# Performance work log

Measured on AMD Instinct MI355X. Metric: run time of the kernel, lower is better.

Reference implementation:

```python
import jax, jax.numpy as jnp
import numpy as np

N, E, E3, DIM = 25000, 50000, 40000, 64


def setup_inputs() -> dict:
    key = jax.random.key(0)
    ks = jax.random.split(key, 16)
    def g(k, shape, scale=0.1):
        return jax.random.normal(k, shape, jnp.float32) * scale
    return {
        "x": jax.random.normal(ks[0], (N, 8), jnp.float32),
        "edge_attr": jax.random.uniform(ks[1], (E, 19), dtype=jnp.float32),
        "edge_attr3": jax.random.uniform(ks[2], (E3, 8), dtype=jnp.float32),
        "edge_index": jax.random.randint(ks[3], (2, E), 0, N),
        "edge_index3": jax.random.randint(ks[4], (2, E3), 0, N),
        "W_node": g(ks[5], (8, DIM)), "b_node": jnp.zeros((DIM,), jnp.float32),
        "W_ea": g(ks[6], (19, 12)), "b_ea": jnp.zeros((12,), jnp.float32),
        "W_e1": g(ks[7], (12, 128)), "b_e1": jnp.zeros((128,), jnp.float32),
        "W_e2": g(ks[8], (128, DIM * DIM), 0.01), "b_e2": jnp.zeros((DIM * DIM,), jnp.float32),
        "conv_bias": jnp.zeros((DIM,), jnp.float32),
        "W_ih": g(ks[9], (3 * DIM, DIM)), "b_ih": jnp.zeros((3 * DIM,), jnp.float32),
        "W_hh": g(ks[10], (3 * DIM, DIM)), "b_hh": jnp.zeros((3 * DIM,), jnp.float32),
        "W_l1": g(ks[11], (DIM + 8, 128)), "b_l1": jnp.zeros((128,), jnp.float32),
        "W_l2": g(ks[12], (128, 1)), "b_l2": jnp.zeros((1,), jnp.float32),
    }


def _forward(x, edge_attr, edge_attr3,
             W_node, b_node, W_ea, b_ea, W_e1, b_e1, W_e2, b_e2, conv_bias,
             W_ih, b_ih, W_hh, b_hh, W_l1, b_l1, W_l2, b_l2,
             edge_index, edge_index3):
    dim = W_node.shape[1]
    n = x.shape[0]
    out = jax.nn.relu(x @ W_node + b_node)                      # [N, dim]
    ea = jax.nn.relu(edge_attr @ W_ea + b_ea)                   # [E, 12]
    # edge MLP -> per-edge dim x dim weight matrices (same for all 3 conv calls)
    Wedge = (jax.nn.relu(ea @ W_e1 + b_e1) @ W_e2 + b_e2).reshape(-1, dim, dim)  # [E, dim, dim]
    src, dst = edge_index[0], edge_index[1]
    ones = jnp.ones((src.shape[0],), x.dtype)
    cnt = jnp.maximum(jax.ops.segment_sum(ones, dst, num_segments=n), 1.0)  # [N]
    h = out
    for _ in range(3):
        msg = jnp.einsum('ed,edf->ef', out[src], Wedge)                     # per-edge GEMV
        agg = jax.ops.segment_sum(msg, dst, num_segments=n) / cnt[:, None]  # scatter-mean
        m = jax.nn.relu(agg + conv_bias)
        # single-step GRU (PyTorch gate order: r, z, n)
        gi = m @ W_ih.T + b_ih
        gh = h @ W_hh.T + b_hh
        ir, iz, inn = jnp.split(gi, 3, axis=-1)
        hr, hz, hn = jnp.split(gh, 3, axis=-1)
        r = jax.nn.sigmoid(ir + hr)
        z = jax.nn.sigmoid(iz + hz)
        ng = jnp.tanh(inn + r * hn)
        h = (1.0 - z) * ng + z * h
        out = h
    pair = (out[edge_index3[0]] + out[edge_index3[1]]) * 0.5    # mean over the 2 endpoints
    yhat = jnp.concatenate([pair, edge_attr3], axis=1)          # [E3, dim+8]
    yhat = jax.nn.relu(yhat @ W_l1 + b_l1) @ W_l2 + b_l2        # [E3, 1]
    return yhat[:, 0]


def reference(x, edge_attr, edge_attr3, edge_index, edge_index3,
              W_node, b_node, W_ea, b_ea, W_e1, b_e1, W_e2, b_e2, conv_bias,
              W_ih, b_ih, W_hh, b_hh, W_l1, b_l1, W_l2, b_l2):
    return _forward(x, edge_attr, edge_attr3,
                    W_node, b_node, W_ea, b_ea, W_e1, b_e1, W_e2, b_e2, conv_bias,
                    W_ih, b_ih, W_hh, b_hh, W_l1, b_l1, W_l2, b_l2,
                    edge_index, edge_index3)
```

## Files before the change

### kernel.cpp

```cpp
#include <hip/hip_runtime.h>

typedef unsigned short u16;
typedef unsigned int u32;
typedef __attribute__((ext_vector_type(8))) short short8v;
typedef __attribute__((ext_vector_type(4))) float float4v;

__device__ __forceinline__ float sigm(float x) { return 1.0f / (1.0f + __expf(-x)); }
__device__ __forceinline__ u16 f2bf(float f) {
  u32 u = __float_as_uint(f);
  u32 r = (u + 0x7fffu + ((u >> 16) & 1u)) >> 16;
  return (u16)r;
}
__device__ __forceinline__ float bf2f(u16 w) { return __uint_as_float(((u32)w) << 16); }

__global__ void k_zero_i(int* __restrict__ p, int n) {
  int i = blockIdx.x * blockDim.x + threadIdx.x;
  if (i < n) p[i] = 0;
}

__global__ void k_cnt(const int* __restrict__ dst, int* __restrict__ cnt, int E) {
  int e = blockIdx.x * blockDim.x + threadIdx.x;
  if (e < E) atomicAdd(&cnt[dst[e]], 1);
}

__global__ void k_scan1(const int* __restrict__ cnt, int* __restrict__ bsum, int N) {
  __shared__ int ws[4];
  int t = threadIdx.x;
  int i = blockIdx.x * 256 + t;
  int v = (i < N) ? cnt[i] : 0;
  int s = v;
  for (int off = 1; off < 64; off <<= 1) s += __shfl_xor(s, off);
  int wid = t >> 6, lane = t & 63;
  if (lane == 0) ws[wid] = s;
  __syncthreads();
  if (t == 0) bsum[blockIdx.x] = ws[0] + ws[1] + ws[2] + ws[3];
}

__global__ void k_scan2(int* __restrict__ bsum, int* __restrict__ row, int nb, int N) {
  __shared__ int s[256];
  int t = threadIdx.x;
  if (t < nb) s[t] = bsum[t];
  __syncthreads();
  if (t == 0) {
    int run = 0;
    for (int i = 0; i < nb; ++i) { int x = s[i]; s[i] = run; run += x; }
    row[N] = run;
  }
  __syncthreads();
  if (t < nb) bsum[t] = s[t];
}

__global__ void k_scan3(const int* __restrict__ cnt, const int* __restrict__ bsum,
                        int* __restrict__ row, int* __restrict__ cursor, int N) {
  __shared__ int ws[4];
  int t = threadIdx.x;
  int i = blockIdx.x * 256 + t;
  int v = (i < N) ? cnt[i] : 0;
  int lane = t & 63, wid = t >> 6;
  int incl = v;
  for (int off = 1; off < 64; off <<= 1) {
    int u = __shfl_up(incl, off);
    if (lane >= off) incl += u;
  }
  if (lane == 63) ws[wid] = incl;
  __syncthreads();
  int woff = bsum[blockIdx.x];
  for (int w = 0; w < wid; ++w) woff += ws[w];
  int excl = woff + incl - v;
  if (i < N) { row[i] = excl; cursor[i] = excl; }
}

__global__ void k_pos(const int* __restrict__ dst, int* __restrict__ cursor,
                      int* __restrict__ pos, int E) {
  int e = blockIdx.x * blockDim.x + threadIdx.x;
  if (e < E) pos[e] = atomicAdd(&cursor[dst[e]], 1);
}

__global__ void k_node(const float* __restrict__ x, const float* __restrict__ Wn,
                       const float* __restrict__ bn, float* __restrict__ h, int N) {
  int tid = blockIdx.x * blockDim.x + threadIdx.x;
  if (tid >= N * 64) return;
  int n = tid >> 6, f = tid & 63;
  float acc = bn[f];
  for (int k = 0; k < 8; ++k) acc += x[(size_t)n * 8 + k] * Wn[k * 64 + f];
  h[tid] = fmaxf(acc, 0.0f);
}

__global__ __launch_bounds__(256) void k_edge_mlp(
    const float* __restrict__ ea_in, const float* __restrict__ Wea,
    const float* __restrict__ bea, const float* __restrict__ We1,
    const float* __restrict__ be1, u16* __restrict__ Ahi, int E) {
  __shared__ float att[2][19];
  __shared__ float ea[2][12];
  int half = threadIdx.x >> 7;
  int t = threadIdx.x & 127;
  int e = blockIdx.x * 2 + half;
  bool real = (e < E);
  int ee = real ? e : E - 1;
  if (t < 19) att[half][t] = ea_in[(size_t)ee * 19 + t];
  __syncthreads();
  if (t < 12) {
    float a = bea[t];
#pragma unroll
    for (int k = 0; k < 19; ++k) a += att[half][k] * Wea[k * 12 + t];
    ea[half][t] = fmaxf(a, 0.0f);
  }
  __syncthreads();
  float a = be1[t];
#pragma unroll
  for (int j = 0; j < 12; ++j) a += ea[half][j] * We1[j * 128 + t];
  if (real) Ahi[(size_t)e * 128 + t] = f2bf(fmaxf(a, 0.0f));
}

__global__ void k_pack_b(const float* __restrict__ W2, u16* __restrict__ Bph) {
  int tid = blockIdx.x * blockDim.x + threadIdx.x;
  if (tid >= 128 * 4096) return;
  int j = tid & 7;
  int lane = (tid >> 3) & 63;
  int nt = (tid >> 9) & 3;
  int ks = (tid >> 11) & 3;
  int d = tid >> 13;
  int c = lane & 15, q = lane >> 4;
  int k = ks * 32 + q * 8 + j;
  int n = d * 64 + nt * 16 + c;
  Bph[tid] = f2bf(W2[(size_t)k * 4096 + n]);
}

__global__ void k_prep_wtf(const float* __restrict__ Wih, const float* __restrict__ Whh,
                           u16* __restrict__ WpI, u16* __restrict__ WpH) {
  int tid = blockIdx.x * blockDim.x + threadIdx.x;
  if (tid >= 2 * 12288) return;
  int w = tid / 12288;
  int r = tid - w * 12288;
  int jj = r & 7;
  int lane = (r >> 3) & 63;
  int t = r >> 9;
  int nt = t % 12, ks = t / 12;
  int c = lane & 15, q = lane >> 4;
  int j = nt * 16 + c;
  int k = ks * 32 + q * 8 + jj;
  const float* W = w ? Whh : Wih;
  u16* Wp = w ? WpH : WpI;
  Wp[r] = f2bf(W[j * 64 + k]);
}

__global__ void k_prep_wl1(const float* __restrict__ Wl1, u16* __restrict__ Wp1) {
  int tid = blockIdx.x * blockDim.x + threadIdx.x;
  if (tid >= 3 * 8 * 64 * 8) return;
  int j = tid & 7;
  int lane = (tid >> 3) & 63;
  int nt = (tid >> 9) & 7;
  int ks = tid >> 12;
  int c = lane & 15, q = lane >> 4;
  int k = ks * 32 + q * 8 + j;
  int n = nt * 16 + c;
  Wp1[tid] = f2bf((k < 72) ? Wl1[k * 128 + n] : 0.0f);
}

__global__ __launch_bounds__(256, 2) void k_conv_fused(
    const u16* __restrict__ Ahi, const u16* __restrict__ Bph,
    const float* __restrict__ b2, const float* __restrict__ h,
    const int* __restrict__ src, const int* __restrict__ pos,
    float* __restrict__ msgp, int E) {
  __shared__ __align__(16) u16 sB[3][8192];
  __shared__ __align__(16) float hsT[32 * 132];
  __shared__ __align__(16) u16 sb2h[4096];
  int m0 = blockIdx.x * 128;
  int tid = threadIdx.x;
  int wave = tid >> 6, lane = tid & 63;
  int mw = wave >> 1, fw = wave & 1;
  int c = lane & 15, q = lane >> 4;

  auto stageB = [&](int d, int b) {
    const u16* gp = Bph + (size_t)d * 8192 + wave * 2048 + lane * 8;
    u16* lp = &sB[b][wave * 2048];
#pragma unroll
    for (int i = 0; i < 4; ++i)
      __builtin_amdgcn_global_load_lds(
          (const __attribute__((address_space(1))) unsigned int*)(gp + i * 512),
          (__attribute__((address_space(3))) unsigned int*)(lp + i * 512), 16, 0, 0);
  };
  auto loadHsT = [&](int dbase) {
#pragma unroll
    for (int p = 0; p < 4; ++p) {
      int slot = p * 256 + tid;
      int r = slot >> 3, s = slot & 7;
      int ge = m0 + r;
      if (ge >= E) ge = E - 1;
      int sn = src[ge];
      float4 v = *(const float4*)(h + (size_t)sn * 64 + dbase + s * 4);
      hsT[(s * 4 + 0) * 132 + r] = v.x;
      hsT[(s * 4 + 1) * 132 + r] = v.y;
      hsT[(s * 4 + 2) * 132 + r] = v.z;
      hsT[(s * 4 + 3) * 132 + r] = v.w;
    }
  };

  stageB(0, 0);
  stageB(1, 1);

  short8v afr[4][4];
#pragma unroll
  for (int mt = 0; mt < 4; ++mt) {
    int gr = m0 + mw * 64 + mt * 16 + c;
    if (gr >= E) gr = E - 1;
    const u16* ap = Ahi + (size_t)gr * 128 + q * 8;
#pragma unroll
    for (int ks = 0; ks < 4; ++ks) afr[mt][ks] = *(const short8v*)(ap + ks * 32);
  }

  loadHsT(0);
  {
    int t16 = tid * 16;
#pragma unroll
    for (int u = 0; u < 4; ++u) {
      float4 v = *(const float4*)(b2 + t16 + u * 4);
      sb2h[t16 + u * 4 + 0] = f2bf(v.x);
      sb2h[t16 + u * 4 + 1] = f2bf(v.y);
      sb2h[t16 + u * 4 + 2] = f2bf(v.z);
      sb2h[t16 + u * 4 + 3] = f2bf(v.w);
    }
  }
  __syncthreads();

  float msg[4][2][4];
#pragma unroll
  for (int mt = 0; mt < 4; ++mt)
#pragma unroll
    for (int nt = 0; nt < 2; ++nt)
#pragma unroll
      for (int r = 0; r < 4; ++r) msg[mt][nt][r] = 0.0f;

  int cur = 0;
  int nx2 = 2;
  for (int dl = 0; dl < 64; ++dl) {
    if (dl < 63) asm volatile("s_waitcnt vmcnt(4)" ::: "memory");
    else         asm volatile("s_waitcnt vmcnt(0)" ::: "memory");
    __builtin_amdgcn_s_barrier();
    asm volatile("" ::: "memory");
    if (dl == 32) {
      loadHsT(32);
      asm volatile("s_waitcnt vmcnt(0) lgkmcnt(0)" ::: "memory");
      __builtin_amdgcn_s_barrier();
      asm volatile("" ::: "memory");
    }
    if (dl < 62) stageB(dl + 2, nx2);

    float b2v0 = bf2f(sb2h[dl * 64 + fw * 32 + c]);
    float b2v1 = bf2f(sb2h[dl * 64 + fw * 32 + 16 + c]);
    float4v acc[4][2];
#pragma unroll
    for (int mt = 0; mt < 4; ++mt)
#pragma unroll
      for (int nt = 0; nt < 2; ++nt) acc[mt][nt] = (float4v){0.f, 0.f, 0.f, 0.f};
    __builtin_amdgcn_s_setprio(1);
#pragma unroll
    for (int ks = 0; ks < 4; ++ks) {
      short8v b0 = *(const short8v*)(&sB[cur][ks * 2048 + fw * 1024 + lane * 8]);
      short8v b1 = *(const short8v*)(&sB[cur][ks * 2048 + fw * 1024 + 512 + lane * 8]);
#pragma unroll
      for (int mt = 0; mt < 4; ++mt) {
        acc[mt][0] = __builtin_amdgcn_mfma_f32_16x16x32_bf16(afr[mt][ks], b0, acc[mt][0], 0, 0, 0);
        acc[mt][1] = __builtin_amdgcn_mfma_f32_16x16x32_bf16(afr[mt][ks], b1, acc[mt][1], 0, 0, 0);
      }
    }
    __builtin_amdgcn_s_setprio(0);
    int dlh = dl & 31;
#pragma unroll
    for (int mt = 0; mt < 4; ++mt) {
      float4 hd4 = *(const float4*)(&hsT[dlh * 132 + mw * 64 + mt * 16 + q * 4]);
      float hd[4] = {hd4.x, hd4.y, hd4.z, hd4.w};
#pragma unroll
      for (int r = 0; r < 4; ++r) {
        msg[mt][0][r] += hd[r] * (acc[mt][0][r] + b2v0);
        msg[mt][1][r] += hd[r] * (acc[mt][1][r] + b2v1);
      }
    }
    cur = (cur == 2) ? 0 : cur + 1;
    nx2 = (nx2 == 2) ? 0 : nx2 + 1;
  }

#pragma unroll
  for (int mt = 0; mt < 4; ++mt) {
#pragma unroll
    for (int r = 0; r < 4; ++r) {
      int e = m0 + mw * 64 + mt * 16 + q * 4 + r;
      if (e < E) {
        int pe = pos[e];
        float* mp = msgp + (size_t)pe * 64 + fw * 32 + c;
#pragma unroll
        for (int nt = 0; nt < 2; ++nt) mp[nt * 16] = msg[mt][nt][r];
      }
    }
  }
}

__global__ __launch_bounds__(256, 2) void k_gru_mfma(
    const float* __restrict__ msgp, const int* __restrict__ row,
    const float* __restrict__ cb, const u16* __restrict__ WpI,
    const u16* __restrict__ WpH, const float* __restrict__ bih,
    const float* __restrict__ bhh, const float* __restrict__ hin,
    float* __restrict__ hout, int N) {
  __shared__ __align__(16) u16 sM[64 * 72];
  __shared__ __align__(16) u16 sH[64 * 72];
  __shared__ __align__(16) float sHf[64 * 68];
  __shared__ int sRow[65];
  int n0 = blockIdx.x * 64;
  int tid = threadIdx.x;
  if (tid < 65) {
    int idx = n0 + tid;
    sRow[tid] = row[(idx <= N) ? idx : N];
  }
  __syncthreads();
  {
    int nl = tid >> 4, fq = tid & 15;
    float4 cbv = *(const float4*)(cb + fq * 4);
#pragma unroll
    for (int pass = 0; pass < 4; ++pass) {
      int n = pass * 16 + nl;
      int gn = n0 + n;
      bool real = (gn < N);
      int b0 = sRow[n], b1 = sRow[n + 1];
      if (!real) b1 = b0;
      float4 av = {0.f, 0.f, 0.f, 0.f};
      for (int j = b0; j < b1; ++j) {
        float4 mv = *(const float4*)(msgp + (size_t)j * 64 + fq * 4);
        av.x += mv.x; av.y += mv.y; av.z += mv.z; av.w += mv.w;
      }
      float cf = fmaxf((float)(b1 - b0), 1.0f);
      int hgn = real ? gn : N - 1;
      float4 hv = *(const float4*)(hin + (size_t)hgn * 64 + fq * 4);
      float m0v = fmaxf(av.x / cf + cbv.x, 0.0f);
      float m1v = fmaxf(av.y / cf + cbv.y, 0.0f);
      float m2v = fmaxf(av.z / cf + cbv.z, 0.0f);
      float m3v = fmaxf(av.w / cf + cbv.w, 0.0f);
      ushort4 mu; mu.x = f2bf(m0v); mu.y = f2bf(m1v); mu.z = f2bf(m2v); mu.w = f2bf(m3v);
      ushort4 hu; hu.x = f2bf(hv.x); hu.y = f2bf(hv.y); hu.z = f2bf(hv.z); hu.w = f2bf(hv.w);
      *(ushort4*)(&sM[n * 72 + fq * 4]) = mu;
      *(ushort4*)(&sH[n * 72 + fq * 4]) = hu;
      *(float4*)(&sHf[n * 68 + fq * 4]) = hv;
    }
  }
  __syncthreads();
  int wave = tid >> 6, lane = tid & 63;
  int c = lane & 15, q = lane >> 4;
  short8v am[2], ah[2];
#pragma unroll
  for (int ks = 0; ks < 2; ++ks) {
    am[ks] = *(const short8v*)(&sM[(wave * 16 + c) * 72 + ks * 32 + q * 8]);
    ah[ks] = *(const short8v*)(&sH[(wave * 16 + c) * 72 + ks * 32 + q * 8]);
  }
  float4v accRZ[8], accN[4], accHN[4];
#pragma unroll
  for (int i = 0; i < 8; ++i) accRZ[i] = (float4v){0.f, 0.f, 0.f, 0.f};
#pragma unroll
  for (int i = 0; i < 4; ++i) {
    accN[i] = (float4v){0.f, 0.f, 0.f, 0.f};
    accHN[i] = (float4v){0.f, 0.f, 0.f, 0.f};
  }
#pragma unroll
  for (int ks = 0; ks < 2; ++ks) {
#pragma unroll
    for (int nt = 0; nt < 8; ++nt) {
      short8v bI = *(const short8v*)(WpI + ((size_t)(ks * 12 + nt) * 64 + lane) * 8);
      short8v bH = *(const short8v*)(WpH + ((size_t)(ks * 12 + nt) * 64 + lane) * 8);
      accRZ[nt] = __builtin_amdgcn_mfma_f32_16x16x32_bf16(am[ks], bI, accRZ[nt], 0, 0, 0);
      accRZ[nt] = __builtin_amdgcn_mfma_f32_16x16x32_bf16(ah[ks], bH, accRZ[nt], 0, 0, 0);
    }
#pragma unroll
    for (int nt = 0; nt < 4; ++nt) {
      short8v bI = *(const short8v*)(WpI + ((size_t)(ks * 12 + 8 + nt) * 64 + lane) * 8);
      short8v bH = *(const short8v*)(WpH + ((size_t)(ks * 12 + 8 + nt) * 64 + lane) * 8);
      accN[nt] = __builtin_amdgcn_mfma_f32_16x16x32_bf16(am[ks], bI, accN[nt], 0, 0, 0);
      accHN[nt] = __builtin_amdgcn_mfma_f32_16x16x32_bf16(ah[ks], bH, accHN[nt], 0, 0, 0);
    }
  }
#pragma unroll
  for (int nt = 0; nt < 4; ++nt) {
    int f = nt * 16 + c;
    float brz_r = bih[f] + bhh[f];
    float brz_z = bih[64 + f] + bhh[64 + f];
    float bin = bih[128 + f];
    float bhn = bhh[128 + f];
#pragma unroll
    for (int r = 0; r < 4; ++r) {
      int nl = wave * 16 + q * 4 + r;
      int gn = n0 + nl;
      float rr = sigm(accRZ[nt][r] + brz_r);
      float zz = sigm(accRZ[nt + 4][r] + brz_z);
      float ng = tanhf(accN[nt][r] + bin + rr * (accHN[nt][r] + bhn));
      float hv = sHf[nl * 68 + f];
      if (gn < N) hout[(size_t)gn * 64 + f] = (1.0f - zz) * ng + zz * hv;
    }
  }
}

__global__ __launch_bounds__(256) void k_final_mfma(
    const float* __restrict__ h, const float* __restrict__ ea3,
    const int* __restrict__ idx3, const u16* __restrict__ Wp1,
    const float* __restrict__ bl1, const float* __restrict__ Wl2,
    const float* __restrict__ bl2, float* __restrict__ out, int E3) {
  __shared__ __align__(16) u16 sF[64 * 104];
  int e0 = blockIdx.x * 64;
  int tid = threadIdx.x;
  {
    int er = tid >> 2;
    int part = tid & 3;
    int ge = e0 + er;
    int gc = (ge < E3) ? ge : E3 - 1;
    int a = idx3[gc], b = idx3[E3 + gc];
    for (int kk = part * 24; kk < part * 24 + 24; ++kk) {
      float v;
      if (kk < 64) v = 0.5f * (h[(size_t)a * 64 + kk] + h[(size_t)b * 64 + kk]);
      else if (kk < 72) v = ea3[(size_t)gc * 8 + (kk - 64)];
      else v = 0.0f;
      sF[er * 104 + kk] = f2bf(v);
    }
  }
  __syncthreads();
  int wave = tid >> 6, lane = tid & 63;
  int c = lane & 15, q = lane >> 4;
  float4v acc[8];
#pragma unroll
  for (int nt = 0; nt < 8; ++nt) acc[nt] = (float4v){0.f, 0.f, 0.f, 0.f};
#pragma unroll
  for (int ks = 0; ks < 3; ++ks) {
    short8v af = *(const short8v*)(&sF[(wave * 16 + c) * 104 + ks * 32 + q * 8]);
#pragma unroll
    for (int nt = 0; nt < 8; ++nt) {
      short8v bf = *(const short8v*)(Wp1 + ((size_t)(ks * 8 + nt) * 64 + lane) * 8);
      acc[nt] = __builtin_amdgcn_mfma_f32_16x16x32_bf16(af, bf, acc[nt], 0, 0, 0);
    }
  }
  float v[4] = {0.f, 0.f, 0.f, 0.f};
#pragma unroll
  for (int nt = 0; nt < 8; ++nt) {
    int n = nt * 16 + c;
    float b1 = bl1[n];
    float w2 = Wl2[n];
#pragma unroll
    for (int r = 0; r < 4; ++r) v[r] += fmaxf(acc[nt][r] + b1, 0.0f) * w2;
  }
#pragma unroll
  for (int off = 1; off < 16; off <<= 1) {
#pragma unroll
    for (int r = 0; r < 4; ++r) v[r] += __shfl_xor(v[r], off);
  }
  if (c == 0) {
    float b2v = bl2[0];
#pragma unroll
    for (int r = 0; r < 4; ++r) {
      int e = e0 + wave * 16 + q * 4 + r;
      if (e < E3) out[e] = v[r] + b2v;
    }
  }
}

extern "C" void kernel_launch(void* const* d_in, const int* in_sizes, int n_in,
                              void* d_out, int out_size, void* d_ws, size_t ws_size,
                              hipStream_t stream) {
  const float* x          = (const float*)d_in[0];
  const float* edge_attr  = (const float*)d_in[1];
  const float* edge_attr3 = (const float*)d_in[2];
  const int*   edge_index = (const int*)d_in[3];
  const int*   edge_index3= (const int*)d_in[4];
  const float* W_node = (const float*)d_in[5];
  const float* b_node = (const float*)d_in[6];
  const float* W_ea   = (const float*)d_in[7];
  const float* b_ea   = (const float*)d_in[8];
  const float* W_e1   = (const float*)d_in[9];
  const float* b_e1   = (const float*)d_in[10];
  const float* W_e2   = (const float*)d_in[11];
  const float* b_e2   = (const float*)d_in[12];
  const float* conv_bias = (const float*)d_in[13];
  const float* W_ih   = (const float*)d_in[14];
  const float* b_ih   = (const float*)d_in[15];
  const float* W_hh   = (const float*)d_in[16];
  const float* b_hh   = (const float*)d_in[17];
  const float* W_l1   = (const float*)d_in[18];
  const float* b_l1   = (const float*)d_in[19];
  const float* W_l2   = (const float*)d_in[20];
  const float* b_l2   = (const float*)d_in[21];

  int N  = in_sizes[0] / 8;
  int E  = in_sizes[1] / 19;
  int E3 = in_sizes[2] / 8;

  char* p = (char*)d_ws;
  auto carve = [&](size_t bytes) -> void* {
    char* q = p;
    p += (bytes + 255) & ~(size_t)255;
    return (void*)q;
  };
  float* hA    = (float*)carve((size_t)N * 64 * 4);
  float* hB    = (float*)carve((size_t)N * 64 * 4);
  float* msgp  = (float*)carve((size_t)E * 64 * 4);
  int*   cnt   = (int*)carve((size_t)N * 4);
  int*   row   = (int*)carve((size_t)(N + 1) * 4);
  int*   cursor= (int*)carve((size_t)N * 4);
  int*   pos   = (int*)carve((size_t)E * 4);
  int*   bsum  = (int*)carve(256 * 4);
  u16*   Ahi   = (u16*)carve((size_t)E * 128 * 2);
  u16*   Bph   = (u16*)carve((size_t)128 * 4096 * 2);
  u16*   WpI   = (u16*)carve(12288 * 2);
  u16*   WpH   = (u16*)carve(12288 * 2);
  u16*   Wp1   = (u16*)carve(12288 * 2);

  const int* src = edge_index;
  const int* dst = edge_index + E;

  int nb = (N + 255) / 256;
  k_zero_i<<<(N + 255) / 256, 256, 0, stream>>>(cnt, N);
  k_cnt<<<(E + 255) / 256, 256, 0, stream>>>(dst, cnt, E);
  k_scan1<<<nb, 256, 0, stream>>>(cnt, bsum, N);
  k_scan2<<<1, 256, 0, stream>>>(bsum, row, nb, N);
  k_scan3<<<nb, 256, 0, stream>>>(cnt, bsum, row, cursor, N);
  k_pos<<<(E + 255) / 256, 256, 0, stream>>>(dst, cursor, pos, E);

  k_node<<<((size_t)N * 64 + 255) / 256, 256, 0, stream>>>(x, W_node, b_node, hA, N);
  k_edge_mlp<<<(E + 1) / 2, 256, 0, stream>>>(edge_attr, W_ea, b_ea, W_e1, b_e1, Ahi, E);
  k_pack_b<<<(128 * 4096 + 255) / 256, 256, 0, stream>>>(W_e2, Bph);
  k_prep_wtf<<<(2 * 12288 + 255) / 256, 256, 0, stream>>>(W_ih, W_hh, WpI, WpH);
  k_prep_wl1<<<(12288 + 255) / 256, 256, 0, stream>>>(W_l1, Wp1);

  float* hcur = hA;
  float* hnxt = hB;
  int gconv = (E + 127) / 128;
  int ngru = (N + 63) / 64;
  for (int it = 0; it < 3; ++it) {
    k_conv_fused<<<gconv, 256, 0, stream>>>(Ahi, Bph, b_e2, hcur, src, pos, msgp, E);
    k_gru_mfma<<<ngru, 256, 0, stream>>>(msgp, row, conv_bias, WpI, WpH,
                                         b_ih, b_hh, hcur, hnxt, N);
    float* tmp = hcur; hcur = hnxt; hnxt = tmp;
  }
  k_final_mfma<<<(E3 + 63) / 64, 256, 0, stream>>>(hcur, edge_attr3, edge_index3, Wp1,
                                                   b_l1, W_l2, b_l2, (float*)d_out, E3);
}
```

Baseline: 424.0 us.

## Split conv over two d-halves, merge prep kernels, vectorize final gather

The fused conv kernel now splits the 64-step inner-dimension loop across a second grid dimension, so each block handles 32 d-values and writes a partial message to a doubled msgp buffer. The GRU then sums the two partials. Per block the B staging drops from triple to double buffering, and b2 is read directly from global memory instead of a converted LDS copy, which frees LDS and allows the launch bound to rise to 3 blocks per CU. The four small prep kernels are merged into one launch, the zero kernel becomes a memset, and the final kernel's pair/feature gather uses float4 loads. The cost is twice the message write traffic, extra reads in the GRU, and a __syncthreads per loop step.

Result: slower. 444.6 us (+4.9%).

```diff
diff --git a/kernel.cpp b/kernel.cpp
--- a/kernel.cpp
+++ b/kernel.cpp
@@ -12,11 +12,6 @@
   return (u16)r;
 }
 __device__ __forceinline__ float bf2f(u16 w) { return __uint_as_float(((u32)w) << 16); }
-
-__global__ void k_zero_i(int* __restrict__ p, int n) {
-  int i = blockIdx.x * blockDim.x + threadIdx.x;
-  if (i < n) p[i] = 0;
-}
 
 __global__ void k_cnt(const int* __restrict__ dst, int* __restrict__ cnt, int E) {
   int e = blockIdx.x * blockDim.x + threadIdx.x;
@@ -74,16 +69,6 @@
                       int* __restrict__ pos, int E) {
   int e = blockIdx.x * blockDim.x + threadIdx.x;
   if (e < E) pos[e] = atomicAdd(&cursor[dst[e]], 1);
-}
-
-__global__ void k_node(const float* __restrict__ x, const float* __restrict__ Wn,
-                       const float* __restrict__ bn, float* __restrict__ h, int N) {
-  int tid = blockIdx.x * blockDim.x + threadIdx.x;
-  if (tid >= N * 64) return;
-  int n = tid >> 6, f = tid & 63;
-  float acc = bn[f];
-  for (int k = 0; k < 8; ++k) acc += x[(size_t)n * 8 + k] * Wn[k * 64 + f];
-  h[tid] = fmaxf(acc, 0.0f);
 }
 
 __global__ __launch_bounds__(256) void k_edge_mlp(
@@ -112,60 +97,71 @@
   if (real) Ahi[(size_t)e * 128 + t] = f2bf(fmaxf(a, 0.0f));
 }
 
-__global__ void k_pack_b(const float* __restrict__ W2, u16* __restrict__ Bph) {
-  int tid = blockIdx.x * blockDim.x + threadIdx.x;
-  if (tid >= 128 * 4096) return;
-  int j = tid & 7;
-  int lane = (tid >> 3) & 63;
-  int nt = (tid >> 9) & 3;
-  int ks = (tid >> 11) & 3;
-  int d = tid >> 13;
-  int c = lane & 15, q = lane >> 4;
-  int k = ks * 32 + q * 8 + j;
-  int n = d * 64 + nt * 16 + c;
-  Bph[tid] = f2bf(W2[(size_t)k * 4096 + n]);
-}
-
-__global__ void k_prep_wtf(const float* __restrict__ Wih, const float* __restrict__ Whh,
-                           u16* __restrict__ WpI, u16* __restrict__ WpH) {
-  int tid = blockIdx.x * blockDim.x + threadIdx.x;
-  if (tid >= 2 * 12288) return;
-  int w = tid / 12288;
-  int r = tid - w * 12288;
-  int jj = r & 7;
-  int lane = (r >> 3) & 63;
-  int t = r >> 9;
-  int nt = t % 12, ks = t / 12;
-  int c = lane & 15, q = lane >> 4;
-  int j = nt * 16 + c;
-  int k = ks * 32 + q * 8 + jj;
-  const float* W = w ? Whh : Wih;
-  u16* Wp = w ? WpH : WpI;
-  Wp[r] = f2bf(W[j * 64 + k]);
-}
-
-__global__ void k_prep_wl1(const float* __restrict__ Wl1, u16* __restrict__ Wp1) {
-  int tid = blockIdx.x * blockDim.x + threadIdx.x;
-  if (tid >= 3 * 8 * 64 * 8) return;
-  int j = tid & 7;
-  int lane = (tid >> 3) & 63;
-  int nt = (tid >> 9) & 7;
-  int ks = tid >> 12;
-  int c = lane & 15, q = lane >> 4;
-  int k = ks * 32 + q * 8 + j;
-  int n = nt * 16 + c;
-  Wp1[tid] = f2bf((k < 72) ? Wl1[k * 128 + n] : 0.0f);
-}
-
-__global__ __launch_bounds__(256, 2) void k_conv_fused(
+__global__ void k_prep_all(
+    const float* __restrict__ x, const float* __restrict__ Wn,
+    const float* __restrict__ bn, float* __restrict__ h, int N, int nbNode,
+    const float* __restrict__ W2, u16* __restrict__ Bph, int nbPack,
+    const float* __restrict__ Wih, const float* __restrict__ Whh,
+    u16* __restrict__ WpI, u16* __restrict__ WpH, int nbWtf,
+    const float* __restrict__ Wl1, u16* __restrict__ Wp1) {
+  int b = blockIdx.x;
+  if (b < nbNode) {
+    int tid = b * 256 + threadIdx.x;
+    if (tid >= N * 64) return;
+    int n = tid >> 6, f = tid & 63;
+    float acc = bn[f];
+    for (int k = 0; k < 8; ++k) acc += x[(size_t)n * 8 + k] * Wn[k * 64 + f];
+    h[tid] = fmaxf(acc, 0.0f);
+  } else if (b < nbNode + nbPack) {
+    int tid = (b - nbNode) * 256 + threadIdx.x;
+    if (tid >= 128 * 4096) return;
+    int j = tid & 7;
+    int lane = (tid >> 3) & 63;
+    int nt = (tid >> 9) & 3;
+    int ks = (tid >> 11) & 3;
+    int d = tid >> 13;
+    int c = lane & 15, q = lane >> 4;
+    int k = ks * 32 + q * 8 + j;
+    int n = d * 64 + nt * 16 + c;
+    Bph[tid] = f2bf(W2[(size_t)k * 4096 + n]);
+  } else if (b < nbNode + nbPack + nbWtf) {
+    int tid = (b - nbNode - nbPack) * 256 + threadIdx.x;
+    if (tid >= 2 * 12288) return;
+    int w = tid / 12288;
+    int r = tid - w * 12288;
+    int jj = r & 7;
+    int lane = (r >> 3) & 63;
+    int t = r >> 9;
+    int nt = t % 12, ks = t / 12;
+    int c = lane & 15, q = lane >> 4;
+    int j = nt * 16 + c;
+    int k = ks * 32 + q * 8 + jj;
+    const float* W = w ? Whh : Wih;
+    u16* Wp = w ? WpH : WpI;
+    Wp[r] = f2bf(W[j * 64 + k]);
+  } else {
+    int tid = (b - nbNode - nbPack - nbWtf) * 256 + threadIdx.x;
+    if (tid >= 3 * 8 * 64 * 8) return;
+    int j = tid & 7;
+    int lane = (tid >> 3) & 63;
+    int nt = (tid >> 9) & 7;
+    int ks = tid >> 12;
+    int c = lane & 15, q = lane >> 4;
+    int k = ks * 32 + q * 8 + j;
+    int n = nt * 16 + c;
+    Wp1[tid] = f2bf((k < 72) ? Wl1[k * 128 + n] : 0.0f);
+  }
+}
+
+__global__ __launch_bounds__(256, 3) void k_conv_fused(
     const u16* __restrict__ Ahi, const u16* __restrict__ Bph,
     const float* __restrict__ b2, const float* __restrict__ h,
     const int* __restrict__ src, const int* __restrict__ pos,
     float* __restrict__ msgp, int E) {
-  __shared__ __align__(16) u16 sB[3][8192];
+  __shared__ __align__(16) u16 sB[2][8192];
   __shared__ __align__(16) float hsT[32 * 132];
-  __shared__ __align__(16) u16 sb2h[4096];
   int m0 = blockIdx.x * 128;
+  int d0 = blockIdx.y * 32;
   int tid = threadIdx.x;
   int wave = tid >> 6, lane = tid & 63;
   int mw = wave >> 1, fw = wave & 1;
@@ -180,24 +176,8 @@
           (const __attribute__((address_space(1))) unsigned int*)(gp + i * 512),
           (__attribute__((address_space(3))) unsigned int*)(lp + i * 512), 16, 0, 0);
   };
-  auto loadHsT = [&](int dbase) {
-#pragma unroll
-    for (int p = 0; p < 4; ++p) {
-      int slot = p * 256 + tid;
-      int r = slot >> 3, s = slot & 7;
-      int ge = m0 + r;
-      if (ge >= E) ge = E - 1;
-      int sn = src[ge];
-      float4 v = *(const float4*)(h + (size_t)sn * 64 + dbase + s * 4);
-      hsT[(s * 4 + 0) * 132 + r] = v.x;
-      hsT[(s * 4 + 1) * 132 + r] = v.y;
-      hsT[(s * 4 + 2) * 132 + r] = v.z;
-      hsT[(s * 4 + 3) * 132 + r] = v.w;
-    }
-  };
-
-  stageB(0, 0);
-  stageB(1, 1);
+
+  stageB(d0, 0);
 
   short8v afr[4][4];
 #pragma unroll
@@ -209,18 +189,21 @@
     for (int ks = 0; ks < 4; ++ks) afr[mt][ks] = *(const short8v*)(ap + ks * 32);
   }
 
-  loadHsT(0);
-  {
-    int t16 = tid * 16;
-#pragma unroll
-    for (int u = 0; u < 4; ++u) {
-      float4 v = *(const float4*)(b2 + t16 + u * 4);
-      sb2h[t16 + u * 4 + 0] = f2bf(v.x);
-      sb2h[t16 + u * 4 + 1] = f2bf(v.y);
-      sb2h[t16 + u * 4 + 2] = f2bf(v.z);
-      sb2h[t16 + u * 4 + 3] = f2bf(v.w);
-    }
-  }
+#pragma unroll
+  for (int p = 0; p < 4; ++p) {
+    int slot = p * 256 + tid;
+    int r = slot >> 3, s = slot & 7;
+    int ge = m0 + r;
+    if (ge >= E) ge = E - 1;
+    int sn = src[ge];
+    float4 v = *(const float4*)(h + (size_t)sn * 64 + d0 + s * 4);
+    hsT[(s * 4 + 0) * 132 + r] = v.x;
+    hsT[(s * 4 + 1) * 132 + r] = v.y;
+    hsT[(s * 4 + 2) * 132 + r] = v.z;
+    hsT[(s * 4 + 3) * 132 + r] = v.w;
+  }
+  float b2v0 = b2[(size_t)d0 * 64 + fw * 32 + c];
+  float b2v1 = b2[(size_t)d0 * 64 + fw * 32 + 16 + c];
   __syncthreads();
 
   float msg[4][2][4];
@@ -232,22 +215,13 @@
       for (int r = 0; r < 4; ++r) msg[mt][nt][r] = 0.0f;
 
   int cur = 0;
-  int nx2 = 2;
-  for (int dl = 0; dl < 64; ++dl) {
-    if (dl < 63) asm volatile("s_waitcnt vmcnt(4)" ::: "memory");
-    else         asm volatile("s_waitcnt vmcnt(0)" ::: "memory");
-    __builtin_amdgcn_s_barrier();
-    asm volatile("" ::: "memory");
-    if (dl == 32) {
-      loadHsT(32);
-      asm volatile("s_waitcnt vmcnt(0) lgkmcnt(0)" ::: "memory");
-      __builtin_amdgcn_s_barrier();
-      asm volatile("" ::: "memory");
-    }
-    if (dl < 62) stageB(dl + 2, nx2);
-
-    float b2v0 = bf2f(sb2h[dl * 64 + fw * 32 + c]);
-    float b2v1 = bf2f(sb2h[dl * 64 + fw * 32 + 16 + c]);
+  for (int dl = 0; dl < 32; ++dl) {
+    float nb0 = 0.f, nb1 = 0.f;
+    if (dl < 31) {
+      stageB(d0 + dl + 1, cur ^ 1);
+      nb0 = b2[(size_t)(d0 + dl + 1) * 64 + fw * 32 + c];
+      nb1 = b2[(size_t)(d0 + dl + 1) * 64 + fw * 32 + 16 + c];
+    }
     float4v acc[4][2];
 #pragma unroll
     for (int mt = 0; mt < 4; ++mt)
@@ -265,10 +239,9 @@
       }
     }
     __builtin_amdgcn_s_setprio(0);
-    int dlh = dl & 31;
 #pragma unroll
     for (int mt = 0; mt < 4; ++mt) {
-      float4 hd4 = *(const float4*)(&hsT[dlh * 132 + mw * 64 + mt * 16 + q * 4]);
+      float4 hd4 = *(const float4*)(&hsT[dl * 132 + mw * 64 + mt * 16 + q * 4]);
       float hd[4] = {hd4.x, hd4.y, hd4.z, hd4.w};
 #pragma unroll
       for (int r = 0; r < 4; ++r) {
@@ -276,8 +249,9 @@
         msg[mt][1][r] += hd[r] * (acc[mt][1][r] + b2v1);
       }
     }
-    cur = (cur == 2) ? 0 : cur + 1;
-    nx2 = (nx2 == 2) ? 0 : nx2 + 1;
+    __syncthreads();
+    b2v0 = nb0; b2v1 = nb1;
+    cur ^= 1;
   }
 
 #pragma unroll
@@ -287,7 +261,7 @@
       int e = m0 + mw * 64 + mt * 16 + q * 4 + r;
       if (e < E) {
         int pe = pos[e];
-        float* mp = msgp + (size_t)pe * 64 + fw * 32 + c;
+        float* mp = msgp + (size_t)pe * 128 + blockIdx.y * 64 + fw * 32 + c;
 #pragma unroll
         for (int nt = 0; nt < 2; ++nt) mp[nt * 16] = msg[mt][nt][r];
       }
@@ -324,8 +298,10 @@
       if (!real) b1 = b0;
       float4 av = {0.f, 0.f, 0.f, 0.f};
       for (int j = b0; j < b1; ++j) {
-        float4 mv = *(const float4*)(msgp + (size_t)j * 64 + fq * 4);
-        av.x += mv.x; av.y += mv.y; av.z += mv.z; av.w += mv.w;
+        float4 m0 = *(const float4*)(msgp + (size_t)j * 128 + fq * 4);
+        float4 m1 = *(const float4*)(msgp + (size_t)j * 128 + 64 + fq * 4);
+        av.x += m0.x + m1.x; av.y += m0.y + m1.y;
+        av.z += m0.z + m1.z; av.w += m0.w + m1.w;
       }
       float cf = fmaxf((float)(b1 - b0), 1.0f);
       int hgn = real ? gn : N - 1;
@@ -409,12 +385,31 @@
     int ge = e0 + er;
     int gc = (ge < E3) ? ge : E3 - 1;
     int a = idx3[gc], b = idx3[E3 + gc];
-    for (int kk = part * 24; kk < part * 24 + 24; ++kk) {
-      float v;
-      if (kk < 64) v = 0.5f * (h[(size_t)a * 64 + kk] + h[(size_t)b * 64 + kk]);
-      else if (kk < 72) v = ea3[(size_t)gc * 8 + (kk - 64)];
-      else v = 0.0f;
-      sF[er * 104 + kk] = f2bf(v);
+    const float* pa = h + (size_t)a * 64 + part * 16;
+    const float* pb = h + (size_t)b * 64 + part * 16;
+#pragma unroll
+    for (int u = 0; u < 4; ++u) {
+      float4 va = *(const float4*)(pa + u * 4);
+      float4 vb = *(const float4*)(pb + u * 4);
+      ushort4 mu;
+      mu.x = f2bf(0.5f * (va.x + vb.x));
+      mu.y = f2bf(0.5f * (va.y + vb.y));
+      mu.z = f2bf(0.5f * (va.z + vb.z));
+      mu.w = f2bf(0.5f * (va.w + vb.w));
+      *(ushort4*)(&sF[er * 104 + part * 16 + u * 4]) = mu;
+    }
+    if (part == 0) {
+      float4 e0v = *(const float4*)(ea3 + (size_t)gc * 8);
+      float4 e1v = *(const float4*)(ea3 + (size_t)gc * 8 + 4);
+      ushort4 u0, u1;
+      u0.x = f2bf(e0v.x); u0.y = f2bf(e0v.y); u0.z = f2bf(e0v.z); u0.w = f2bf(e0v.w);
+      u1.x = f2bf(e1v.x); u1.y = f2bf(e1v.y); u1.z = f2bf(e1v.z); u1.w = f2bf(e1v.w);
+      *(ushort4*)(&sF[er * 104 + 64]) = u0;
+      *(ushort4*)(&sF[er * 104 + 68]) = u1;
+    } else {
+      ushort4 z = {0, 0, 0, 0};
+      *(ushort4*)(&sF[er * 104 + 72 + (part - 1) * 8]) = z;
+      *(ushort4*)(&sF[er * 104 + 76 + (part - 1) * 8]) = z;
     }
   }
   __syncthreads();
@@ -494,7 +489,7 @@
   };
   float* hA    = (float*)carve((size_t)N * 64 * 4);
   float* hB    = (float*)carve((size_t)N * 64 * 4);
-  float* msgp  = (float*)carve((size_t)E * 64 * 4);
+  float* msgp  = (float*)carve((size_t)E * 128 * 4);
   int*   cnt   = (int*)carve((size_t)N * 4);
   int*   row   = (int*)carve((size_t)(N + 1) * 4);
   int*   cursor= (int*)carve((size_t)N * 4);
@@ -510,22 +505,25 @@
   const int* dst = edge_index + E;
 
   int nb = (N + 255) / 256;
-  k_zero_i<<<(N + 255) / 256, 256, 0, stream>>>(cnt, N);
+  hipMemsetAsync(cnt, 0, (size_t)N * 4, stream);
   k_cnt<<<(E + 255) / 256, 256, 0, stream>>>(dst, cnt, E);
   k_scan1<<<nb, 256, 0, stream>>>(cnt, bsum, N);
   k_scan2<<<1, 256, 0, stream>>>(bsum, row, nb, N);
   k_scan3<<<nb, 256, 0, stream>>>(cnt, bsum, row, cursor, N);
   k_pos<<<(E + 255) / 256, 256, 0, stream>>>(dst, cursor, pos, E);
 
-  k_node<<<((size_t)N * 64 + 255) / 256, 256, 0, stream>>>(x, W_node, b_node, hA, N);
   k_edge_mlp<<<(E + 1) / 2, 256, 0, stream>>>(edge_attr, W_ea, b_ea, W_e1, b_e1, Ahi, E);
-  k_pack_b<<<(128 * 4096 + 255) / 256, 256, 0, stream>>>(W_e2, Bph);
-  k_prep_wtf<<<(2 * 12288 + 255) / 256, 256, 0, stream>>>(W_ih, W_hh, WpI, WpH);
-  k_prep_wl1<<<(12288 + 255) / 256, 256, 0, stream>>>(W_l1, Wp1);
+  int nbNode = ((size_t)N * 64 + 255) / 256;
+  int nbPack = (128 * 4096 + 255) / 256;
+  int nbWtf  = (2 * 12288 + 255) / 256;
+  int nbWl1  = (12288 + 255) / 256;
+  k_prep_all<<<nbNode + nbPack + nbWtf + nbWl1, 256, 0, stream>>>(
+      x, W_node, b_node, hA, N, nbNode, W_e2, Bph, nbPack,
+      W_ih, W_hh, WpI, WpH, nbWtf, W_l1, Wp1);
 
   float* hcur = hA;
   float* hnxt = hB;
-  int gconv = (E + 127) / 128;
+  dim3 gconv((E + 127) / 128, 2);
   int ngru = (N + 63) / 64;
   for (int it = 0; it < 3; ++it) {
     k_conv_fused<<<gconv, 256, 0, stream>>>(Ahi, Bph, b_e2, hcur, src, pos, msgp, E);
```
